# Kernel optimization log

Measured on AMD Instinct MI355X. Metric: run time of the kernel, lower is better.

The kernel has to match this reference:

```python
import jax, jax.numpy as jnp
import numpy as np
import math

B, T, C, F = 8, 2048, 1024, 4096
N_LAYER, LAYER_ID = 12, 1


def _init_params(key):
    ks = jax.random.split(key, 16)
    s = 0.02
    ratio_0_to_1 = LAYER_ID / (N_LAYER - 1)
    ratio_1_to_almost0 = 1.0 - LAYER_ID / N_LAYER
    h = np.arange(C, dtype=np.float32)
    decay = -5.0 + 8.0 * (h / (C - 1)) ** (0.7 + 1.3 * ratio_0_to_1)
    zigzag = np.array([((i + 1) % 3 - 1) for i in range(C)], dtype=np.float32) * 0.5
    first = np.ones(C, dtype=np.float32) * math.log(0.3) + zigzag
    xi = (np.arange(C, dtype=np.float32) / C)
    p = {
        'ln1_w': jnp.ones(C), 'ln1_b': jnp.zeros(C),
        'ln2_w': jnp.ones(C), 'ln2_b': jnp.zeros(C),
        'att_time_decay': jnp.asarray(decay),
        'att_time_first': jnp.asarray(first),
        'att_mix_k': jnp.asarray(xi ** ratio_1_to_almost0),
        'att_mix_v': jnp.asarray(xi ** ratio_1_to_almost0 + 0.3 * ratio_0_to_1),
        'att_mix_r': jnp.asarray(xi ** (0.5 * ratio_1_to_almost0)),
        'att_Wk': jax.random.normal(ks[0], (C, C)) * s,
        'att_Wv': jax.random.normal(ks[1], (C, C)) * s,
        'att_Wr': jax.random.normal(ks[2], (C, C)) * s,
        'att_Wo': jax.random.normal(ks[3], (C, C)) * s,
        'ffn_mix_k': jnp.asarray(xi ** ratio_1_to_almost0),
        'ffn_mix_r': jnp.asarray(xi ** ratio_1_to_almost0),
        'ffn_Wk': jax.random.normal(ks[4], (F, C)) * s,
        'ffn_Wr': jax.random.normal(ks[5], (C, C)) * s,
        'ffn_Wv': jax.random.normal(ks[6], (C, F)) * s,
        'short_W': jax.random.normal(ks[7], (C, C)) * s,
    }
    return p


def setup_inputs() -> dict:
    key = jax.random.key(0)
    k1, k2 = jax.random.split(key)
    inp = {'x': jax.random.normal(k1, (B, T, C), dtype=jnp.float32)}
    inp.update(_init_params(k2))
    return inp


def _layernorm(x, w, b, eps=1e-5):
    mu = jnp.mean(x, axis=-1, keepdims=True)
    var = jnp.var(x, axis=-1, keepdims=True)
    return (x - mu) * jax.lax.rsqrt(var + eps) * w + b


def _time_shift(x):
    # ZeroPad2d((0,0,1,-1)): prepend zero row along T, drop last
    return jnp.pad(x, ((0, 0), (1, 0), (0, 0)))[:, :-1]


def _wkv(time_decay, time_first, k, v):
    # numerically-stable WKV recurrence, matching the CUDA kernel math
    w = -jnp.exp(time_decay)  # [C]
    u = time_first            # [C]
    kt = jnp.swapaxes(k, 0, 1)  # [T,B,C]
    vt = jnp.swapaxes(v, 0, 1)
    a0 = jnp.zeros(k.shape[::2] if False else (k.shape[0], k.shape[2]), k.dtype)
    b0 = jnp.zeros_like(a0)
    p0 = jnp.full_like(a0, -1e30)

    def step(carry, kv):
        a, b, p = carry
        k_t, v_t = kv
        ww = u + k_t
        q = jnp.maximum(p, ww)
        e1 = jnp.exp(p - q)
        e2 = jnp.exp(ww - q)
        y = (e1 * a + e2 * v_t) / (e1 * b + e2)
        ww2 = p + w
        q2 = jnp.maximum(ww2, k_t)
        f1 = jnp.exp(ww2 - q2)
        f2 = jnp.exp(k_t - q2)
        return (f1 * a + f2 * v_t, f1 * b + f2, q2), y

    _, ys = jax.lax.scan(step, (a0, b0, p0), (kt, vt))
    return jnp.swapaxes(ys, 0, 1)  # [B,T,C]


def _lin(x, W):
    return jnp.einsum('btc,oc->bto', x, W)


def reference(x, ln1_w, ln1_b, ln2_w, ln2_b,
              att_time_decay, att_time_first, att_mix_k, att_mix_v, att_mix_r,
              att_Wk, att_Wv, att_Wr, att_Wo,
              ffn_mix_k, ffn_mix_r, ffn_Wk, ffn_Wr, ffn_Wv, short_W):
    # --- TimeMix on ln1(x) ---
    h = _layernorm(x, ln1_w, ln1_b)
    hh = _time_shift(h)
    xk = h * att_mix_k + hh * (1 - att_mix_k)
    xv = h * att_mix_v + hh * (1 - att_mix_v)
    xr = h * att_mix_r + hh * (1 - att_mix_r)
    k = _lin(xk, att_Wk)
    v = _lin(xv, att_Wv)
    sr = jax.nn.sigmoid(_lin(xr, att_Wr))
    rwkv = sr * _wkv(att_time_decay, att_time_first, k, v)
    att_out = _lin(rwkv, att_Wo)
    # shortcut linear replaces identity residual (L3TC Block)
    x = _lin(x, short_W) + att_out
    # --- ChannelMix on ln2(x) ---
    g = _layernorm(x, ln2_w, ln2_b)
    gg = _time_shift(g)
    gk = g * ffn_mix_k + gg * (1 - ffn_mix_k)
    gr = g * ffn_mix_r + gg * (1 - ffn_mix_r)
    kk = jnp.square(jax.nn.relu(_lin(gk, ffn_Wk)))
    kv = _lin(kk, ffn_Wv)
    rkv = jax.nn.sigmoid(_lin(gr, ffn_Wr)) * kv
    return x + rkv
```

## Files before the change

kernel.cpp:

```cpp
#include <hip/hip_runtime.h>

#define BB 8
#define TT 2048
#define CC 1024
#define FF 4096
#define MM (BB*TT)

typedef unsigned short u16;
typedef __bf16 bf16x8 __attribute__((ext_vector_type(8)));
typedef float f32x4 __attribute__((ext_vector_type(4)));

__device__ __forceinline__ u16 f2bf(float f) {
  unsigned int u = __float_as_uint(f);
  u += 0x7fffu + ((u >> 16) & 1u);
  return (u16)(u >> 16);
}
__device__ __forceinline__ float bf2f(u16 h) {
  unsigned int u = ((unsigned int)h) << 16;
  return __uint_as_float(u);
}
__device__ __forceinline__ float sigm(float x) { return 1.f / (1.f + __expf(-x)); }

__device__ __forceinline__ void async16(const void* g, void* l) {
  __builtin_amdgcn_global_load_lds(
      (const __attribute__((address_space(1))) unsigned int*)g,
      (__attribute__((address_space(3))) unsigned int*)l, 16, 0, 0);
}

template<int MODE>
__global__ __launch_bounds__(256, 2) void gemm_bt(
    const u16* __restrict__ A, const u16* __restrict__ W,
    float* __restrict__ Cf, u16* __restrict__ Cb, int N, int K)
{
  __shared__ __align__(16) u16 ldsA[128 * 32];
  __shared__ __align__(16) u16 ldsB[128 * 32];
  const int tid  = threadIdx.x;
  const int wave = tid >> 6;
  const int lane = tid & 63;
  const int bm = blockIdx.x * 128;
  const int bn = blockIdx.y * 128;
  const int wm = (wave >> 1) * 64;
  const int wn = (wave & 1) * 64;
  const int lm = lane & 15;
  const int lq = lane >> 4;

  const int r_in = lane >> 2;
  const int cp   = lane & 3;
  const int cg   = cp ^ ((r_in >> 1) & 3);
  const int rA0  = wave * 16 + r_in;
  const int rA1  = 64 + rA0;
  const u16* gA0 = A + (size_t)(bm + rA0) * K + cg * 8;
  const u16* gA1 = A + (size_t)(bm + rA1) * K + cg * 8;
  const u16* gB0 = W + (size_t)(bn + rA0) * K + cg * 8;
  const u16* gB1 = W + (size_t)(bn + rA1) * K + cg * 8;
  u16* lA0 = &ldsA[(wave * 16) * 32];
  u16* lA1 = &ldsA[(64 + wave * 16) * 32];
  u16* lB0 = &ldsB[(wave * 16) * 32];
  u16* lB1 = &ldsB[(64 + wave * 16) * 32];

  const int crd  = lq ^ ((lm >> 1) & 3);
  const int offA0 = (wm + lm) * 32 + crd * 8;
  const int offB0 = (wn + lm) * 32 + crd * 8;

  f32x4 acc[4][4] = {};

  for (int kt = 0; kt < K; kt += 32) {
    async16(gA0 + kt, lA0);
    async16(gA1 + kt, lA1);
    async16(gB0 + kt, lB0);
    async16(gB1 + kt, lB1);
    __syncthreads();
    bf16x8 bfr[4];
#pragma unroll
    for (int ni = 0; ni < 4; ++ni)
      bfr[ni] = *(const bf16x8*)&ldsB[offB0 + ni * 16 * 32];
#pragma unroll
    for (int mi = 0; mi < 4; ++mi) {
      bf16x8 afr = *(const bf16x8*)&ldsA[offA0 + mi * 16 * 32];
#pragma unroll
      for (int ni = 0; ni < 4; ++ni)
        acc[mi][ni] = __builtin_amdgcn_mfma_f32_16x16x32_bf16(afr, bfr[ni], acc[mi][ni], 0, 0, 0);
    }
    __syncthreads();
  }

  const int row0 = bm + wm + lq * 4;
  const int col0 = bn + wn + lm;
#pragma unroll
  for (int mi = 0; mi < 4; ++mi)
#pragma unroll
    for (int ni = 0; ni < 4; ++ni) {
      size_t base = (size_t)(row0 + mi * 16) * N + (col0 + ni * 16);
#pragma unroll
      for (int r2 = 0; r2 < 4; ++r2) {
        size_t idx = base + (size_t)r2 * N;
        float v = acc[mi][ni][r2];
        if (MODE == 0) Cf[idx] = v;
        if (MODE == 1) Cf[idx] += v;
        if (MODE == 2) { float rl = v > 0.f ? v : 0.f; Cb[idx] = f2bf(rl * rl); }
        if (MODE == 3) Cb[idx] = f2bf(v);
      }
    }
}

__global__ __launch_bounds__(256) void prep_mix(
    const float* __restrict__ x,
    const float* __restrict__ lnw, const float* __restrict__ lnb,
    const float* __restrict__ mk, const float* __restrict__ mv, const float* __restrict__ mr,
    u16* __restrict__ ok, u16* __restrict__ ov, u16* __restrict__ orr,
    u16* __restrict__ oxb)
{
  const int m = blockIdx.x;
  const int t = m & (TT - 1);
  const int tid = threadIdx.x;
  const int wave = tid >> 6, lane = tid & 63;
  const bool hasp = (t != 0);

  const float4 xc4 = ((const float4*)(x + (size_t)m * CC))[tid];
  float4 xp4 = make_float4(0.f, 0.f, 0.f, 0.f);
  if (hasp) xp4 = ((const float4*)(x + (size_t)(m - 1) * CC))[tid];

  float s0 = xc4.x + xc4.y + xc4.z + xc4.w;
  float s1 = xc4.x*xc4.x + xc4.y*xc4.y + xc4.z*xc4.z + xc4.w*xc4.w;
  float s2 = xp4.x + xp4.y + xp4.z + xp4.w;
  float s3 = xp4.x*xp4.x + xp4.y*xp4.y + xp4.z*xp4.z + xp4.w*xp4.w;
#pragma unroll
  for (int off2 = 32; off2 > 0; off2 >>= 1) {
    s0 += __shfl_xor(s0, off2);
    s1 += __shfl_xor(s1, off2);
    s2 += __shfl_xor(s2, off2);
    s3 += __shfl_xor(s3, off2);
  }
  __shared__ float red[4][4];
  if (lane == 0) { red[0][wave] = s0; red[1][wave] = s1; red[2][wave] = s2; red[3][wave] = s3; }
  __syncthreads();
  const float S0 = red[0][0] + red[0][1] + red[0][2] + red[0][3];
  const float S1 = red[1][0] + red[1][1] + red[1][2] + red[1][3];
  const float S2 = red[2][0] + red[2][1] + red[2][2] + red[2][3];
  const float S3 = red[3][0] + red[3][1] + red[3][2] + red[3][3];
  const float inv = 1.f / (float)CC;
  const float muc = S0 * inv, varc = S1 * inv - muc * muc, rsc = rsqrtf(varc + 1e-5f);
  const float mup = S2 * inv, varp = S3 * inv - mup * mup, rsp = rsqrtf(varp + 1e-5f);

  const float xc[4] = {xc4.x, xc4.y, xc4.z, xc4.w};
  const float xp[4] = {xp4.x, xp4.y, xp4.z, xp4.w};
  const float4 lw4 = ((const float4*)lnw)[tid];
  const float4 lb4 = ((const float4*)lnb)[tid];
  const float lw[4] = {lw4.x, lw4.y, lw4.z, lw4.w};
  const float lb[4] = {lb4.x, lb4.y, lb4.z, lb4.w};
  const float4 mk4 = ((const float4*)mk)[tid];
  const float mka[4] = {mk4.x, mk4.y, mk4.z, mk4.w};
  const float4 mr4 = ((const float4*)mr)[tid];
  const float mra[4] = {mr4.x, mr4.y, mr4.z, mr4.w};
  float mva[4] = {0.f, 0.f, 0.f, 0.f};
  if (ov) {
    const float4 mv4 = ((const float4*)mv)[tid];
    mva[0] = mv4.x; mva[1] = mv4.y; mva[2] = mv4.z; mva[3] = mv4.w;
  }

  ushort4 wk2, wv2, wr2, wb2;
  u16* pk = (u16*)&wk2; u16* pv = (u16*)&wv2; u16* pr = (u16*)&wr2; u16* pb = (u16*)&wb2;
#pragma unroll
  for (int j = 0; j < 4; ++j) {
    float h  = (xc[j] - muc) * rsc * lw[j] + lb[j];
    float hh = hasp ? (xp[j] - mup) * rsp * lw[j] + lb[j] : 0.f;
    pk[j] = f2bf(h * mka[j] + hh * (1.f - mka[j]));
    pv[j] = f2bf(h * mva[j] + hh * (1.f - mva[j]));
    pr[j] = f2bf(h * mra[j] + hh * (1.f - mra[j]));
    pb[j] = f2bf(xc[j]);
  }
  ((ushort4*)(ok + (size_t)m * CC))[tid] = wk2;
  if (ov)  ((ushort4*)(ov  + (size_t)m * CC))[tid] = wv2;
  ((ushort4*)(orr + (size_t)m * CC))[tid] = wr2;
  if (oxb) ((ushort4*)(oxb + (size_t)m * CC))[tid] = wb2;
}

#define WKV_CPB 32
#define WKV_NCH 32
#define WKV_L   (TT / WKV_NCH)

__global__ __launch_bounds__(1024) void wkv_scan(
    const u16* __restrict__ k, const u16* __restrict__ v, const u16* __restrict__ r,
    const float* __restrict__ decay, const float* __restrict__ first,
    u16* __restrict__ out)
{
  const int b  = blockIdx.x >> 5;
  const int c0 = (blockIdx.x & 31) * WKV_CPB;
  const int tid = threadIdx.x;
  const int cl = tid & 31;
  const int j  = tid >> 5;
  const int c  = c0 + cl;

  const float w    = -__expf(decay[c]);
  const float lam  = __expf(w);
  const float eu   = __expf(first[c]);
  const float LamL = __expf(w * (float)WKV_L);

  const size_t base = (size_t)b * TT * CC + (size_t)j * WKV_L * CC + c;

  float a = 0.f, bb = 0.f;
  size_t idx = base;
  for (int i = 0; i < WKV_L; ++i, idx += CC) {
    const float kt = bf2f(k[idx]), vt = bf2f(v[idx]);
    const float ek = __expf(kt);
    a  = fmaf(lam, a, ek * vt);
    bb = fmaf(lam, bb, ek);
  }

  __shared__ float sA[WKV_NCH][WKV_CPB];
  __shared__ float sB[WKV_NCH][WKV_CPB];
  sA[j][cl] = a; sB[j][cl] = bb;
  __syncthreads();
  if (tid < WKV_CPB) {
    float ca = 0.f, cb = 0.f;
    const float cw   = -__expf(decay[c0 + tid]);
    const float cLam = __expf(cw * (float)WKV_L);
#pragma unroll
    for (int q = 0; q < WKV_NCH; ++q) {
      const float ta = sA[q][tid], tb = sB[q][tid];
      sA[q][tid] = ca; sB[q][tid] = cb;
      ca = fmaf(cLam, ca, ta);
      cb = fmaf(cLam, cb, tb);
    }
  }
  __syncthreads();
  a = sA[j][cl]; bb = sB[j][cl];

  idx = base;
  for (int i = 0; i < WKV_L; ++i, idx += CC) {
    const float kt = bf2f(k[idx]), vt = bf2f(v[idx]), rt = bf2f(r[idx]);
    const float ek = __expf(kt);
    const float e2 = eu * ek;
    const float y  = (a + e2 * vt) / (bb + e2);
    out[idx] = f2bf(sigm(rt) * y);
    a  = fmaf(lam, a, ek * vt);
    bb = fmaf(lam, bb, ek);
  }
}

struct ConvArgs { const float* src[8]; int end[8]; };

__global__ __launch_bounds__(256) void conv_w(ConvArgs args, u16* __restrict__ dst)
{
  const int i = (blockIdx.x * 256 + threadIdx.x) * 4;
  const float* sp = args.src[0];
  int base = 0;
#pragma unroll
  for (int s = 1; s < 8; ++s) {
    if (i >= args.end[s - 1]) { sp = args.src[s]; base = args.end[s - 1]; }
  }
  const float4 vv = *(const float4*)(sp + (i - base));
  ushort4 d;
  d.x = f2bf(vv.x); d.y = f2bf(vv.y); d.z = f2bf(vv.z); d.w = f2bf(vv.w);
  *(ushort4*)(dst + i) = d;
}

__global__ __launch_bounds__(256) void final_add(
    float* __restrict__ out, const u16* __restrict__ rr, const u16* __restrict__ kv)
{
  const int i = blockIdx.x * 256 + threadIdx.x;
  float4 o = ((const float4*)out)[i];
  const ushort4 r4 = ((const ushort4*)rr)[i];
  const ushort4 k4 = ((const ushort4*)kv)[i];
  o.x += sigm(bf2f(r4.x)) * bf2f(k4.x);
  o.y += sigm(bf2f(r4.y)) * bf2f(k4.y);
  o.z += sigm(bf2f(r4.z)) * bf2f(k4.z);
  o.w += sigm(bf2f(r4.w)) * bf2f(k4.w);
  ((float4*)out)[i] = o;
}

extern "C" void kernel_launch(void* const* d_in, const int* in_sizes, int n_in,
                              void* d_out, int out_size, void* d_ws, size_t ws_size,
                              hipStream_t stream)
{
  const float* x    = (const float*)d_in[0];
  const float* ln1w = (const float*)d_in[1];
  const float* ln1b = (const float*)d_in[2];
  const float* ln2w = (const float*)d_in[3];
  const float* ln2b = (const float*)d_in[4];
  const float* tdec = (const float*)d_in[5];
  const float* tfir = (const float*)d_in[6];
  const float* amk  = (const float*)d_in[7];
  const float* amv  = (const float*)d_in[8];
  const float* amr  = (const float*)d_in[9];
  const float* Wk   = (const float*)d_in[10];
  const float* Wv   = (const float*)d_in[11];
  const float* Wr   = (const float*)d_in[12];
  const float* Wo   = (const float*)d_in[13];
  const float* fmk  = (const float*)d_in[14];
  const float* fmr  = (const float*)d_in[15];
  const float* WfK  = (const float*)d_in[16];
  const float* WfR  = (const float*)d_in[17];
  const float* WfV  = (const float*)d_in[18];
  const float* Wsh  = (const float*)d_in[19];
  float* out = (float*)d_out;
  char* ws = (char*)d_ws;

  u16* wW = (u16*)(ws);
  u16* R0 = (u16*)(ws + 29360128);
  u16* R1 = (u16*)(ws + 62914560);
  u16* R2 = (u16*)(ws + 96468992);
  u16* R3 = (u16*)(ws + 130023424);
  u16* R4 = (u16*)(ws + 163577856);
  u16* R5 = (u16*)(ws + 197132288);

  u16* xk   = R0;
  u16* xv   = R1;
  u16* xr   = R2;
  u16* xb   = R3;
  u16* kbuf = R4;
  u16* vbuf = R0;
  u16* rbuf = R1;
  u16* rwkv = R2;
  u16* gk   = R4;
  u16* gr   = R5;
  u16* kkb  = R0;
  u16* rffn = R4;
  u16* kvb  = R5;

  u16* bWk  = wW + 0;
  u16* bWv  = wW + 1048576;
  u16* bWr  = wW + 2097152;
  u16* bWo  = wW + 3145728;
  u16* bWsh = wW + 4194304;
  u16* bWfR = wW + 5242880;
  u16* bWfK = wW + 6291456;
  u16* bWfV = wW + 10485760;

  ConvArgs ca;
  ca.src[0] = Wk;  ca.src[1] = Wv;  ca.src[2] = Wr;  ca.src[3] = Wo;
  ca.src[4] = Wsh; ca.src[5] = WfR; ca.src[6] = WfK; ca.src[7] = WfV;
  const int e = 1048576;
  ca.end[0] = e;     ca.end[1] = 2*e;  ca.end[2] = 3*e;  ca.end[3] = 4*e;
  ca.end[4] = 5*e;   ca.end[5] = 6*e;  ca.end[6] = 10*e; ca.end[7] = 14*e;

  conv_w<<<14336, 256, 0, stream>>>(ca, wW);
  prep_mix<<<MM, 256, 0, stream>>>(x, ln1w, ln1b, amk, amv, amr, xk, xv, xr, xb);

  dim3 g8(MM / 128, CC / 128);
  gemm_bt<3><<<g8, 256, 0, stream>>>(xk, bWk, nullptr, kbuf, CC, CC);
  gemm_bt<3><<<g8, 256, 0, stream>>>(xv, bWv, nullptr, vbuf, CC, CC);
  gemm_bt<3><<<g8, 256, 0, stream>>>(xr, bWr, nullptr, rbuf, CC, CC);

  wkv_scan<<<BB * (CC / WKV_CPB), 1024, 0, stream>>>(kbuf, vbuf, rbuf, tdec, tfir, rwkv);

  gemm_bt<0><<<g8, 256, 0, stream>>>(xb, bWsh, out, nullptr, CC, CC);
  gemm_bt<1><<<g8, 256, 0, stream>>>(rwkv, bWo, out, nullptr, CC, CC);

  prep_mix<<<MM, 256, 0, stream>>>(out, ln2w, ln2b, fmk, nullptr, fmr, gk, nullptr, gr, nullptr);

  dim3 gF(MM / 128, FF / 128);
  gemm_bt<2><<<gF, 256, 0, stream>>>(gk, bWfK, nullptr, kkb, FF, CC);
  gemm_bt<3><<<g8, 256, 0, stream>>>(gr, bWfR, nullptr, rffn, CC, CC);
  gemm_bt<3><<<g8, 256, 0, stream>>>(kkb, bWfV, nullptr, kvb, CC, FF);

  final_add<<<MM * CC / 1024, 256, 0, stream>>>(out, rffn, kvb);
}
```

Baseline: 958.1 us.

## Concatenate shortcut and output GEMMs, fuse final gating into GEMM epilogue, group-swizzle tiles

Places x_bf16 and the WKV output side by side in one [M,2C] buffer and concatenates Wsh and Wo along K, so one K=2048 GEMM replaces the separate shortcut and output-projection GEMMs and the read-modify-write of out. The final sigmoid-gated residual add moves into the epilogue of the last FFN GEMM (mode 4), which removes the final_add kernel and the kv bf16 intermediate. It also adds a grouped block-index swizzle (GROUP_M=16) meant to improve L2 reuse across tiles. The costs are a strided layout for the concatenated activations and an epilogue that does extra loads and sigmoid work per output.

```diff
diff --git a/kernel.cpp b/kernel.cpp
--- a/kernel.cpp
+++ b/kernel.cpp
@@ -27,18 +27,27 @@
       (__attribute__((address_space(3))) unsigned int*)l, 16, 0, 0);
 }
 
+#define GROUP_M 16
+
 template<int MODE>
-__global__ __launch_bounds__(256, 2) void gemm_bt(
+__device__ __forceinline__ void gemm_body(
     const u16* __restrict__ A, const u16* __restrict__ W,
-    float* __restrict__ Cf, u16* __restrict__ Cb, int N, int K)
+    float* __restrict__ Cf, u16* __restrict__ Cb,
+    const u16* __restrict__ R, int N, int K)
 {
   __shared__ __align__(16) u16 ldsA[128 * 32];
   __shared__ __align__(16) u16 ldsB[128 * 32];
   const int tid  = threadIdx.x;
   const int wave = tid >> 6;
   const int lane = tid & 63;
-  const int bm = blockIdx.x * 128;
-  const int bn = blockIdx.y * 128;
+
+  const int bid  = blockIdx.x + blockIdx.y * gridDim.x;
+  const int gsz  = GROUP_M * gridDim.y;
+  const int gid  = bid / gsz;
+  const int rem  = bid - gid * gsz;
+  const int bm   = (gid * GROUP_M + (rem % GROUP_M)) * 128;
+  const int bn   = (rem / GROUP_M) * 128;
+
   const int wm = (wave >> 1) * 64;
   const int wn = (wave & 1) * 64;
   const int lm = lane & 15;
@@ -96,11 +105,20 @@
         size_t idx = base + (size_t)r2 * N;
         float v = acc[mi][ni][r2];
         if (MODE == 0) Cf[idx] = v;
-        if (MODE == 1) Cf[idx] += v;
         if (MODE == 2) { float rl = v > 0.f ? v : 0.f; Cb[idx] = f2bf(rl * rl); }
         if (MODE == 3) Cb[idx] = f2bf(v);
+        if (MODE == 4) Cf[idx] += sigm(bf2f(R[idx])) * v;
       }
     }
+}
+
+template<int MODE>
+__global__ __launch_bounds__(256, 2) void gemm_bt(
+    const u16* __restrict__ A, const u16* __restrict__ W,
+    float* __restrict__ Cf, u16* __restrict__ Cb,
+    const u16* __restrict__ R, int N, int K)
+{
+  gemm_body<MODE>(A, W, Cf, Cb, R, N, K);
 }
 
 __global__ __launch_bounds__(256) void prep_mix(
@@ -172,7 +190,7 @@
   ((ushort4*)(ok + (size_t)m * CC))[tid] = wk2;
   if (ov)  ((ushort4*)(ov  + (size_t)m * CC))[tid] = wv2;
   ((ushort4*)(orr + (size_t)m * CC))[tid] = wr2;
-  if (oxb) ((ushort4*)(oxb + (size_t)m * CC))[tid] = wb2;
+  if (oxb) ((ushort4*)(oxb + (size_t)m * (2 * CC)))[tid] = wb2;
 }
 
 #define WKV_CPB 32
@@ -191,12 +209,12 @@
   const int j  = tid >> 5;
   const int c  = c0 + cl;
 
-  const float w    = -__expf(decay[c]);
-  const float lam  = __expf(w);
-  const float eu   = __expf(first[c]);
-  const float LamL = __expf(w * (float)WKV_L);
-
-  const size_t base = (size_t)b * TT * CC + (size_t)j * WKV_L * CC + c;
+  const float w   = -__expf(decay[c]);
+  const float lam = __expf(w);
+  const float eu  = __expf(first[c]);
+
+  const size_t base  = (size_t)b * TT * CC + (size_t)j * WKV_L * CC + c;
+  size_t obase = ((size_t)b * TT + (size_t)j * WKV_L) * (2 * CC) + c;
 
   float a = 0.f, bb = 0.f;
   size_t idx = base;
@@ -227,46 +245,38 @@
   a = sA[j][cl]; bb = sB[j][cl];
 
   idx = base;
-  for (int i = 0; i < WKV_L; ++i, idx += CC) {
+  for (int i = 0; i < WKV_L; ++i, idx += CC, obase += 2 * CC) {
     const float kt = bf2f(k[idx]), vt = bf2f(v[idx]), rt = bf2f(r[idx]);
     const float ek = __expf(kt);
     const float e2 = eu * ek;
     const float y  = (a + e2 * vt) / (bb + e2);
-    out[idx] = f2bf(sigm(rt) * y);
+    out[obase] = f2bf(sigm(rt) * y);
     a  = fmaf(lam, a, ek * vt);
     bb = fmaf(lam, bb, ek);
   }
 }
 
-struct ConvArgs { const float* src[8]; int end[8]; };
+struct ConvArgs { const float* src[8]; int end[8]; int dstoff[8]; };
 
 __global__ __launch_bounds__(256) void conv_w(ConvArgs args, u16* __restrict__ dst)
 {
   const int i = (blockIdx.x * 256 + threadIdx.x) * 4;
+  int seg = 0;
   const float* sp = args.src[0];
   int base = 0;
 #pragma unroll
   for (int s = 1; s < 8; ++s) {
-    if (i >= args.end[s - 1]) { sp = args.src[s]; base = args.end[s - 1]; }
-  }
-  const float4 vv = *(const float4*)(sp + (i - base));
+    if (i >= args.end[s - 1]) { seg = s; sp = args.src[s]; base = args.end[s - 1]; }
+  }
+  const int l = i - base;
+  const float4 vv = *(const float4*)(sp + l);
+  int dsti;
+  if (seg == 3)      { int row = l >> 10, col = l & 1023; dsti = args.dstoff[3] + row * 2048 + 1024 + col; }
+  else if (seg == 4) { int row = l >> 10, col = l & 1023; dsti = args.dstoff[4] + row * 2048 + col; }
+  else               dsti = args.dstoff[seg] + l;
   ushort4 d;
   d.x = f2bf(vv.x); d.y = f2bf(vv.y); d.z = f2bf(vv.z); d.w = f2bf(vv.w);
-  *(ushort4*)(dst + i) = d;
-}
-
-__global__ __launch_bounds__(256) void final_add(
-    float* __restrict__ out, const u16* __restrict__ rr, const u16* __restrict__ kv)
-{
-  const int i = blockIdx.x * 256 + threadIdx.x;
-  float4 o = ((const float4*)out)[i];
-  const ushort4 r4 = ((const ushort4*)rr)[i];
-  const ushort4 k4 = ((const ushort4*)kv)[i];
-  o.x += sigm(bf2f(r4.x)) * bf2f(k4.x);
-  o.y += sigm(bf2f(r4.y)) * bf2f(k4.y);
-  o.z += sigm(bf2f(r4.z)) * bf2f(k4.z);
-  o.w += sigm(bf2f(r4.w)) * bf2f(k4.w);
-  ((float4*)out)[i] = o;
+  *(ushort4*)(dst + dsti) = d;
 }
 
 extern "C" void kernel_launch(void* const* d_in, const int* in_sizes, int n_in,
@@ -297,35 +307,31 @@
   char* ws = (char*)d_ws;
 
   u16* wW = (u16*)(ws);
-  u16* R0 = (u16*)(ws + 29360128);
-  u16* R1 = (u16*)(ws + 62914560);
-  u16* R2 = (u16*)(ws + 96468992);
-  u16* R3 = (u16*)(ws + 130023424);
-  u16* R4 = (u16*)(ws + 163577856);
-  u16* R5 = (u16*)(ws + 197132288);
-
-  u16* xk   = R0;
-  u16* xv   = R1;
-  u16* xr   = R2;
-  u16* xb   = R3;
-  u16* kbuf = R4;
-  u16* vbuf = R0;
-  u16* rbuf = R1;
-  u16* rwkv = R2;
-  u16* gk   = R4;
-  u16* gr   = R5;
-  u16* kkb  = R0;
-  u16* rffn = R4;
-  u16* kvb  = R5;
-
-  u16* bWk  = wW + 0;
-  u16* bWv  = wW + 1048576;
-  u16* bWr  = wW + 2097152;
-  u16* bWo  = wW + 3145728;
-  u16* bWsh = wW + 4194304;
-  u16* bWfR = wW + 5242880;
-  u16* bWfK = wW + 6291456;
-  u16* bWfV = wW + 10485760;
+  u16* U0 = (u16*)(ws + 29360128);
+  u16* U1 = (u16*)(ws + 62914560);
+  u16* U2 = (u16*)(ws + 96468992);
+  u16* U3 = (u16*)(ws + 130023424);
+  u16* U4 = (u16*)(ws + 163577856);
+
+  u16* xk   = U0;
+  u16* xv   = U1;
+  u16* xr   = U2;
+  u16* Ap   = U4;
+  u16* kbuf = U3;
+  u16* vbuf = U0;
+  u16* rbuf = U1;
+  u16* gk   = U0;
+  u16* gr   = U1;
+  u16* kkb  = U2;
+  u16* rffn = U0;
+
+  u16* bWk   = wW + 0;
+  u16* bWv   = wW + 1048576;
+  u16* bWr   = wW + 2097152;
+  u16* bWsWo = wW + 3145728;
+  u16* bWfR  = wW + 5242880;
+  u16* bWfK  = wW + 6291456;
+  u16* bWfV  = wW + 10485760;
 
   ConvArgs ca;
   ca.src[0] = Wk;  ca.src[1] = Wv;  ca.src[2] = Wr;  ca.src[3] = Wo;
@@ -333,26 +339,26 @@
   const int e = 1048576;
   ca.end[0] = e;     ca.end[1] = 2*e;  ca.end[2] = 3*e;  ca.end[3] = 4*e;
   ca.end[4] = 5*e;   ca.end[5] = 6*e;  ca.end[6] = 10*e; ca.end[7] = 14*e;
+  ca.dstoff[0] = 0;     ca.dstoff[1] = e;    ca.dstoff[2] = 2*e;
+  ca.dstoff[3] = 3*e;   ca.dstoff[4] = 3*e;
+  ca.dstoff[5] = 5*e;   ca.dstoff[6] = 6*e;  ca.dstoff[7] = 10*e;
 
   conv_w<<<14336, 256, 0, stream>>>(ca, wW);
-  prep_mix<<<MM, 256, 0, stream>>>(x, ln1w, ln1b, amk, amv, amr, xk, xv, xr, xb);
+  prep_mix<<<MM, 256, 0, stream>>>(x, ln1w, ln1b, amk, amv, amr, xk, xv, xr, Ap);
 
   dim3 g8(MM / 128, CC / 128);
-  gemm_bt<3><<<g8, 256, 0, stream>>>(xk, bWk, nullptr, kbuf, CC, CC);
-  gemm_bt<3><<<g8, 256, 0, stream>>>(xv, bWv, nullptr, vbuf, CC, CC);
-  gemm_bt<3><<<g8, 256, 0, stream>>>(xr, bWr, nullptr, rbuf, CC, CC);
-
-  wkv_scan<<<BB * (CC / WKV_CPB), 1024, 0, stream>>>(kbuf, vbuf, rbuf, tdec, tfir, rwkv);
-
-  gemm_bt<0><<<g8, 256, 0, stream>>>(xb, bWsh, out, nullptr, CC, CC);
-  gemm_bt<1><<<g8, 256, 0, stream>>>(rwkv, bWo, out, nullptr, CC, CC);
+  gemm_bt<3><<<g8, 256, 0, stream>>>(xk, bWk, nullptr, kbuf, nullptr, CC, CC);
+  gemm_bt<3><<<g8, 256, 0, stream>>>(xv, bWv, nullptr, vbuf, nullptr, CC, CC);
+  gemm_bt<3><<<g8, 256, 0, stream>>>(xr, bWr, nullptr, rbuf, nullptr, CC, CC);
+
+  wkv_scan<<<BB * (CC / WKV_CPB), 1024, 0, stream>>>(kbuf, vbuf, rbuf, tdec, tfir, Ap + CC);
+
+  gemm_bt<0><<<g8, 256, 0, stream>>>(Ap, bWsWo, out, nullptr, nullptr, CC, 2 * CC);
 
   prep_mix<<<MM, 256, 0, stream>>>(out, ln2w, ln2b, fmk, nullptr, fmr, gk, nullptr, gr, nullptr);
 
   dim3 gF(MM / 128, FF / 128);
-  gemm_bt<2><<<gF, 256, 0, stream>>>(gk, bWfK, nullptr, kkb, FF, CC);
-  gemm_bt<3><<<g8, 256, 0, stream>>>(gr, bWfR, nullptr, rffn, CC, CC);
-  gemm_bt<3><<<g8, 256, 0, stream>>>(kkb, bWfV, nullptr, kvb, CC, FF);
-
-  final_add<<<MM * CC / 1024, 256, 0, stream>>>(out, rffn, kvb);
-}
+  gemm_bt<2><<<gF, 256, 0, stream>>>(gk, bWfK, nullptr, kkb, nullptr, FF, CC);
+  gemm_bt<3><<<g8, 256, 0, stream>>>(gr, bWfR, nullptr, rffn, nullptr, CC, CC);
+  gemm_bt<4><<<g8, 256, 0, stream>>>(kkb, bWfV, out, nullptr, rffn, CC, FF);
+}
```

New measurement: 887.9 us. 1.08x faster.
